# Optimization experiments

Measured on AMD Instinct MI355X. Metric: run time of the kernel, lower is better.

The kernel has to match this reference:

```python
import jax, jax.numpy as jnp
import numpy as np

N = 30000   # nodes
E = 240000  # edges
G = 16      # graphs in batch
DIMS = [1, 256, 512, 1024]
OUT = 1024

def _xavier(key, fan_in, fan_out):
    lim = float(np.sqrt(6.0 / (fan_in + fan_out)))
    return jax.random.uniform(key, (fan_in, fan_out), minval=-lim, maxval=lim, dtype=jnp.float32)

def setup_inputs() -> dict:
    key = jax.random.key(0)
    ks = jax.random.split(key, 8)
    x = jax.random.normal(ks[0], (N, DIMS[0]), dtype=jnp.float32)
    edge_index = jax.random.randint(ks[1], (2, E), 0, N, dtype=jnp.int64)
    batch = jnp.sort(jax.random.randint(ks[2], (N,), 0, G, dtype=jnp.int64))
    W1 = _xavier(ks[3], DIMS[0], DIMS[1]); b1 = jnp.zeros((DIMS[1],), jnp.float32)
    W2 = _xavier(ks[4], DIMS[1], DIMS[2]); b2 = jnp.zeros((DIMS[2],), jnp.float32)
    W3 = _xavier(ks[5], DIMS[2], DIMS[3]); b3 = jnp.zeros((DIMS[3],), jnp.float32)
    Wo = _xavier(ks[6], DIMS[3], OUT);     bo = jnp.zeros((OUT,), jnp.float32)
    return {"x": x, "edge_index": edge_index, "batch": batch,
            "W1": W1, "b1": b1, "W2": W2, "b2": b2, "W3": W3, "b3": b3,
            "Wo": Wo, "bo": bo}

def reference(x, edge_index, batch, W1, b1, W2, b2, W3, b3, Wo, bo):
    n = x.shape[0]
    loops = jnp.arange(n)
    # GCNConv adds self-loops, then symmetric deg^-1/2 normalization
    src = jnp.concatenate([edge_index[0], loops])
    dst = jnp.concatenate([edge_index[1], loops])
    deg = jnp.zeros((n,), jnp.float32).at[dst].add(1.0)  # >=1 due to self-loops
    dis = jax.lax.rsqrt(deg)
    norm = (dis[src] * dis[dst])[:, None]  # [E+N, 1]

    def gcn(h, W, b):
        h = h @ W                                   # linear (no bias in lin)
        agg = jnp.zeros_like(h).at[dst].add(h[src] * norm)  # scatter-add messages
        return agg + b                              # GCNConv bias

    h = jax.nn.relu(gcn(x, W1, b1))
    h = jax.nn.relu(gcn(h, W2, b2))
    h = jax.nn.relu(gcn(h, W3, b3))
    # global mean pool over graphs
    sums = jnp.zeros((G, h.shape[1]), h.dtype).at[batch].add(h)
    cnt = jnp.zeros((G,), h.dtype).at[batch].add(1.0)
    pooled = sums / jnp.maximum(cnt, 1.0)[:, None]
    return pooled @ Wo + bo
```

## Files before the change

kernel.cpp:

```cpp
#include <hip/hip_runtime.h>
#include <hip/hip_bf16.h>
#include <stdint.h>

#define N_NODES 30000
#define E_EDGES 240000
#define NGRAPH  16
#define D1      256
#define D2      512
#define D3      1024
#define DOUT    1024
#define M_PAD   30720
#define CAP     40

typedef unsigned short ushort_t;
typedef short short8 __attribute__((ext_vector_type(8)));
typedef float f32x4 __attribute__((ext_vector_type(4)));

__device__ __forceinline__ float bf2f(ushort_t u) {
    union { unsigned int i; float f; } v; v.i = ((unsigned int)u) << 16; return v.f;
}
__device__ __forceinline__ ushort_t f2bf(float x) {
    union { float f; unsigned int i; } v; v.f = x;
    unsigned int r = v.i + 0x7fffu + ((v.i >> 16) & 1u);
    return (ushort_t)(r >> 16);
}

__device__ __forceinline__ void gl_lds16(const ushort_t* g, ushort_t* l) {
    __builtin_amdgcn_global_load_lds(
        (const __attribute__((address_space(1))) void*)(g),
        (__attribute__((address_space(3))) void*)(l), 16, 0, 0);
}

__global__ void k_detect(const void* w1, const void* ei, int* flags) {
    int lane = threadIdx.x & 63;
    const ushort_t* h = (const ushort_t*)w1;
    float v = fabsf(bf2f(h[lane * 2]));
    unsigned long long badf = __ballot(!(v <= 0.25f));
    const int* e = (const int*)ei;
    unsigned long long badi = __ballot(e[lane * 2 + 1] != 0);
    if (threadIdx.x == 0) {
        flags[0] = (badf == 0ull) ? 1 : 0;
        flags[1] = (badi == 0ull) ? 1 : 0;
    }
}

__global__ void k_setup(const void* x, const void* batch, const void* w1, const void* b1,
                        const void* b2, const void* b3, const void* bo,
                        const void* W2, const void* W3,
                        float* xf, int* batch32, float* W1f, float* b1f, float* b2f,
                        float* b3f, float* bof, ushort_t* Wt2, ushort_t* Wt3,
                        int* slotcnt, float* pooled, float* pooled2, const int* flags) {
    int isbf = flags[0];
    int bid = blockIdx.x;
    int tid = threadIdx.x;
    if (bid < 492) {
        int i = bid * 256 + tid;
        if (i < 3072) {
            const void* src; float* dst; int idx;
            if      (i < 256)  { src = w1; dst = W1f; idx = i; }
            else if (i < 512)  { src = b1; dst = b1f; idx = i - 256; }
            else if (i < 1024) { src = b2; dst = b2f; idx = i - 512; }
            else if (i < 2048) { src = b3; dst = b3f; idx = i - 1024; }
            else               { src = bo; dst = bof; idx = i - 2048; }
            dst[idx] = isbf ? bf2f(((const ushort_t*)src)[idx]) : ((const float*)src)[idx];
        } else if (i < 33072) {
            int idx = i - 3072;
            xf[idx] = isbf ? bf2f(((const ushort_t*)x)[idx]) : ((const float*)x)[idx];
        } else if (i < 63072) {
            int idx = i - 33072;
            batch32[idx] = flags[1] ? (int)((const long long*)batch)[idx]
                                    : ((const int*)batch)[idx];
        } else if (i < 93072) {
            slotcnt[i - 63072] = 0;
        } else if (i < 109456) {
            pooled[i - 93072] = 0.0f;
        } else if (i < 125840) {
            pooled2[i - 109456] = 0.0f;
        }
    } else {
        __shared__ ushort_t tile[32][33];
        int tb = bid - 492;
        const void* in; ushort_t* out; int R, C, bx, by;
        if (tb < 128) { in = W2; out = Wt2; R = D1; C = D2; bx = tb & 15; by = tb >> 4; }
        else { tb -= 128; in = W3; out = Wt3; R = D2; C = D3; bx = tb & 31; by = tb >> 5; }
        int tx = tid & 31, ty = tid >> 5;
        int c0 = bx * 32, r0 = by * 32;
        for (int i = ty; i < 32; i += 8) {
            size_t idx = (size_t)(r0 + i) * C + c0 + tx;
            tile[i][tx] = isbf ? ((const ushort_t*)in)[idx] : f2bf(((const float*)in)[idx]);
        }
        __syncthreads();
        for (int i = ty; i < 32; i += 8) out[(size_t)(c0 + i) * R + r0 + tx] = tile[tx][i];
    }
}

__global__ void k_edge_count(const void* ei, int* slotcnt, int* slots, const int* flags) {
    int e = blockIdx.x * 256 + threadIdx.x;
    if (e >= E_EDGES) return;
    int s, d;
    if (flags[1]) {
        s = (int)((const long long*)ei)[e];
        d = (int)((const long long*)ei)[E_EDGES + e];
    } else {
        s = ((const int*)ei)[e];
        d = ((const int*)ei)[E_EDGES + e];
    }
    if ((unsigned)s >= N_NODES || (unsigned)d >= N_NODES) return;
    int pos = atomicAdd(&slotcnt[d], 1);
    if (pos < CAP) slots[d * CAP + pos] = s;
}

__global__ void k_s1(const float* xf, const int* slotcnt, const int* slots,
                     const int* batch, float* dis, float* s1, float* cntg) {
    int b = blockIdx.x;
    if (b == 118) {
        int g = threadIdx.x;
        if (g >= NGRAPH) return;
        int lo0 = 0, hi0 = N_NODES;
        while (lo0 < hi0) { int m = (lo0 + hi0) >> 1; if (batch[m] < g) lo0 = m + 1; else hi0 = m; }
        int lo1 = lo0, hi1 = N_NODES;
        while (lo1 < hi1) { int m = (lo1 + hi1) >> 1; if (batch[m] < g + 1) lo1 = m + 1; else hi1 = m; }
        cntg[g] = (float)(lo1 - lo0);
        return;
    }
    int d = b * 256 + threadIdx.x;
    if (d >= N_NODES) return;
    int cd = slotcnt[d];
    float di = rsqrtf(1.0f + (float)cd);
    dis[d] = di;
    int cnt = cd < CAP ? cd : CAP;
    float acc = xf[d] * di;
    for (int k = 0; k < cnt; k++) {
        int s = slots[d * CAP + k];
        acc += xf[s] * rsqrtf(1.0f + (float)slotcnt[s]);
    }
    s1[d] = acc * di;
}

__global__ void k_agg1(const float* s1, const float* W1f, const float* b1f,
                       ushort_t* a2, const int* slots, const int* slotcnt, const float* dis) {
    int node = blockIdx.x * 4 + (threadIdx.x >> 6);
    int lane = threadIdx.x & 63;
    int c4 = lane * 4;
    float w[4], bb[4], a[4];
    #pragma unroll
    for (int j = 0; j < 4; j++) { w[j] = W1f[c4 + j]; bb[j] = b1f[c4 + j]; }
    float di = dis[node];
    int cnt = slotcnt[node]; cnt = cnt < CAP ? cnt : CAP;
    float sv = s1[node];
    float wsl = di * di;
    #pragma unroll
    for (int j = 0; j < 4; j++) a[j] = wsl * fmaxf(sv * w[j] + bb[j], 0.0f);
    for (int k = 0; k < cnt; k++) {
        int s = slots[node * CAP + k];
        float ss = s1[s];
        float wn = dis[s] * di;
        #pragma unroll
        for (int j = 0; j < 4; j++) a[j] += wn * fmaxf(ss * w[j] + bb[j], 0.0f);
    }
    uint2 o;
    o.x = (unsigned int)f2bf(a[0]) | ((unsigned int)f2bf(a[1]) << 16);
    o.y = (unsigned int)f2bf(a[2]) | ((unsigned int)f2bf(a[3]) << 16);
    *(uint2*)&a2[(size_t)node * D1 + c4] = o;
}

__global__ void k_agg2(const ushort_t* h, ushort_t* out, const int* slots,
                       const int* slotcnt, const float* dis) {
    int node = blockIdx.x * 4 + (threadIdx.x >> 6);
    int lane = threadIdx.x & 63;
    int c8 = lane * 8;
    float di = dis[node];
    int cnt = slotcnt[node]; cnt = cnt < CAP ? cnt : CAP;
    float w = di * di;
    const ushort_t* hp = h + c8;
    short8 p = *(const short8*)&hp[(size_t)node * D2];
    float a[8];
    #pragma unroll
    for (int j = 0; j < 8; j++) a[j] = w * bf2f((ushort_t)p[j]);
    if (cnt > 0) {
        int s0 = slots[node * CAP];
        short8 q0 = *(const short8*)&hp[(size_t)s0 * D2];
        float ws0 = dis[s0] * di;
        for (int k = 1; k < cnt; k++) {
            int s1i = slots[node * CAP + k];
            short8 q1 = *(const short8*)&hp[(size_t)s1i * D2];
            float ws1 = dis[s1i] * di;
            #pragma unroll
            for (int j = 0; j < 8; j++) a[j] += ws0 * bf2f((ushort_t)q0[j]);
            q0 = q1; ws0 = ws1;
        }
        #pragma unroll
        for (int j = 0; j < 8; j++) a[j] += ws0 * bf2f((ushort_t)q0[j]);
    }
    uint4 o;
    o.x = (unsigned int)f2bf(a[0]) | ((unsigned int)f2bf(a[1]) << 16);
    o.y = (unsigned int)f2bf(a[2]) | ((unsigned int)f2bf(a[3]) << 16);
    o.z = (unsigned int)f2bf(a[4]) | ((unsigned int)f2bf(a[5]) << 16);
    o.w = (unsigned int)f2bf(a[6]) | ((unsigned int)f2bf(a[7]) << 16);
    *(uint4*)&out[(size_t)node * D2 + c8] = o;
}

#define GPHASE(M0, M1, USTAGE, TAILWAIT)                                               \
    a0 = rdA(slot, M0, inrow0); a1 = rdA(slot, M0, inrow1);                            \
    a2r = rdA(slot, M1, inrow0); a3r = rdA(slot, M1, inrow1);                          \
    if (hn) stage_unit(nslot, t + 1, USTAGE);                                          \
    asm volatile("" ::: "memory");                                                     \
    __builtin_amdgcn_s_barrier();                                                      \
    asm volatile("s_waitcnt lgkmcnt(0)" ::: "memory");                                 \
    __builtin_amdgcn_sched_barrier(0);                                                 \
    __builtin_amdgcn_s_setprio(1);                                                     \
    _Pragma("unroll")                                                                  \
    for (int n = 0; n < 4; ++n) {                                                      \
        acc[M0][n] = __builtin_amdgcn_mfma_f32_16x16x32_bf16(a0,  bf_[n][0], acc[M0][n], 0, 0, 0); \
        acc[M0][n] = __builtin_amdgcn_mfma_f32_16x16x32_bf16(a1,  bf_[n][1], acc[M0][n], 0, 0, 0); \
        acc[M1][n] = __builtin_amdgcn_mfma_f32_16x16x32_bf16(a2r, bf_[n][0], acc[M1][n], 0, 0, 0); \
        acc[M1][n] = __builtin_amdgcn_mfma_f32_16x16x32_bf16(a3r, bf_[n][1], acc[M1][n], 0, 0, 0); \
    }                                                                                  \
    __builtin_amdgcn_s_setprio(0);                                                     \
    TAILWAIT                                                                           \
    asm volatile("" ::: "memory");                                                     \
    __builtin_amdgcn_s_barrier();

#define TW_NONE
#define TW_P2 if (hn) { asm volatile("s_waitcnt vmcnt(4)" ::: "memory"); } \
              else    { asm volatile("s_waitcnt vmcnt(0)" ::: "memory"); }
#define TW_P4 if (hn) { asm volatile("s_waitcnt vmcnt(2)" ::: "memory"); } \
              else    { asm volatile("s_waitcnt vmcnt(0)" ::: "memory"); }

template<int POOL>
__global__ __launch_bounds__(512, 2) void k_gemm8(const ushort_t* A, const ushort_t* Bt,
                                                  const float* bias, const int* batch,
                                                  float* pooled, ushort_t* Cmat,
                                                  int K, int Ncols, int ntn, int NT) {
    __shared__ __align__(16) ushort_t As[2][256 * 64];
    __shared__ __align__(16) ushort_t Bs[2][256 * 64];
    const int tid = threadIdx.x;
    const int id = blockIdx.x;
    const int xcd = id & 7, q = id >> 3;
    const int rt = xcd * ((M_PAD / 256) / 8) + q / ntn;
    const int ct = q % ntn;
    const int bm0 = rt * 256, bn0 = ct * 256;
    const int wave = tid >> 6, lane = tid & 63;
    const int wr = wave >> 2, wc = wave & 3;
    const int l15 = lane & 15, quad = lane >> 4;

    const ushort_t* gA = A + (size_t)bm0 * K;
    const ushort_t* gB = Bt + (size_t)bn0 * K;

    auto stage_blk = [&](ushort_t* ldsbase, const ushort_t* gbase, int kt, int b) {
        int row = b >> 3;
        int kb = (b & 7) ^ (row & 7);
        gl_lds16(gbase + (size_t)row * K + (kt << 6) + (kb << 3), ldsbase + (b << 3));
    };
    auto stage_unit = [&](int slot, int kt, int u) {
        if (u == 0)      { stage_blk(Bs[slot], gB, kt, tid);        stage_blk(Bs[slot], gB, kt, tid + 512); }
        else if (u == 1) { stage_blk(Bs[slot], gB, kt, tid + 1024); stage_blk(Bs[slot], gB, kt, tid + 1536); }
        else if (u == 2) { stage_blk(As[slot], gA, kt, tid);        stage_blk(As[slot], gA, kt, tid + 1024); }
        else             { stage_blk(As[slot], gA, kt, tid + 512);  stage_blk(As[slot], gA, kt, tid + 1536); }
    };

    const int swzx = (l15 & 7) << 4;
    const int inrow0 = (quad * 16) ^ swzx;
    const int inrow1 = (quad * 16 + 64) ^ swzx;
    const int arowb = (wr * 128 + l15) * 128;
    const int browb = (wc * 64 + l15) * 128;

    auto rdA = [&](int slot, int m, int inr) -> short8 {
        return *(const short8*)((const char*)As[slot] + arowb + m * 2048 + inr);
    };
    auto rdB = [&](int slot, int n, int inr) -> short8 {
        return *(const short8*)((const char*)Bs[slot] + browb + n * 2048 + inr);
    };

    stage_unit(0, 0, 0); stage_unit(0, 0, 1); stage_unit(0, 0, 2); stage_unit(0, 0, 3);
    asm volatile("s_waitcnt vmcnt(2)" ::: "memory");
    __builtin_amdgcn_s_barrier();

    f32x4 acc[8][4];
    #pragma unroll
    for (int a = 0; a < 8; a++)
        #pragma unroll
        for (int b = 0; b < 4; b++)
            acc[a][b] = (f32x4){0.f, 0.f, 0.f, 0.f};

    short8 bf_[4][2];
    for (int t = 0; t < NT; ++t) {
        const int slot = t & 1, nslot = slot ^ 1;
        const bool hn = (t + 1) < NT;
        short8 a0, a1, a2r, a3r;
        #pragma unroll
        for (int n = 0; n < 4; ++n) {
            bf_[n][0] = rdB(slot, n, inrow0);
            bf_[n][1] = rdB(slot, n, inrow1);
        }
        GPHASE(0, 1, 0, TW_NONE)
        GPHASE(2, 3, 1, TW_P2)
        GPHASE(4, 5, 2, TW_NONE)
        GPHASE(6, 7, 3, TW_P4)
    }

    if (POOL == 0) {
        #pragma unroll
        for (int im = 0; im < 8; im++) {
            int row = bm0 + wr * 128 + im * 16 + quad * 4;
            #pragma unroll
            for (int in = 0; in < 4; in++) {
                int col = bn0 + wc * 64 + in * 16 + l15;
                float bv = bias[col];
                #pragma unroll
                for (int r = 0; r < 4; r++) {
                    float v = acc[im][in][r] + bv;
                    v = v > 0.0f ? v : 0.0f;
                    Cmat[(size_t)(row + r) * Ncols + col] = f2bf(v);
                }
            }
        }
    } else {
        asm volatile("s_waitcnt vmcnt(0) lgkmcnt(0)" ::: "memory");
        __syncthreads();
        float* pl = (float*)&As[0][0];
        int* gtile = (int*)&Bs[0][0];
        for (int i = tid; i < NGRAPH * 256; i += 512) pl[i] = 0.0f;
        if (tid < 256) {
            int r = bm0 + tid; if (r > N_NODES - 1) r = N_NODES - 1;
            int g = batch[r]; g = g < 0 ? 0 : (g > NGRAPH - 1 ? NGRAPH - 1 : g);
            gtile[tid] = g;
        }
        __syncthreads();

        int gmin = gtile[0], gmax = gtile[255];
        if (gmin == gmax && bm0 + 255 < N_NODES) {
            float csum[4];
            float bv[4];
            #pragma unroll
            for (int in = 0; in < 4; in++) {
                csum[in] = 0.0f;
                bv[in] = bias[bn0 + wc * 64 + in * 16 + l15];
            }
            #pragma unroll
            for (int im = 0; im < 8; im++) {
                #pragma unroll
                for (int in = 0; in < 4; in++) {
                    #pragma unroll
                    for (int r = 0; r < 4; r++)
                        csum[in] += fmaxf(acc[im][in][r] + bv[in], 0.0f);
                }
            }
            #pragma unroll
            for (int in = 0; in < 4; in++) {
                csum[in] += __shfl_xor(csum[in], 16);
                csum[in] += __shfl_xor(csum[in], 32);
            }
            if (quad == 0) {
                #pragma unroll
                for (int in = 0; in < 4; in++)
                    atomicAdd(&pl[gmin * 256 + wc * 64 + in * 16 + l15], csum[in]);
            }
        } else {
            #pragma unroll
            for (int im = 0; im < 8; im++) {
                int rl = wr * 128 + im * 16 + quad * 4;
                #pragma unroll
                for (int in = 0; in < 4; in++) {
                    int cl = wc * 64 + in * 16 + l15;
                    float bv = bias[bn0 + cl];
                    float vsum = 0.0f;
                    int gprev = gtile[rl];
                    #pragma unroll
                    for (int r = 0; r < 4; r++) {
                        int row = bm0 + rl + r;
                        float v = (row < N_NODES) ? fmaxf(acc[im][in][r] + bv, 0.0f) : 0.0f;
                        int g = gtile[rl + r];
                        if (g != gprev) {
                            atomicAdd(&pl[gprev * 256 + cl], vsum);
                            vsum = 0.0f; gprev = g;
                        }
                        vsum += v;
                    }
                    atomicAdd(&pl[gprev * 256 + cl], vsum);
                }
            }
        }
        __syncthreads();

        int span = (gmax - gmin + 1) * 256;
        for (int idx = tid; idx < span; idx += 512) {
            int g = gmin + (idx >> 8), cl = idx & 255;
            float v = pl[g * 256 + cl];
            if (v != 0.0f) atomicAdd(&pooled[g * DOUT + bn0 + cl], v);
        }
    }
}

__global__ __launch_bounds__(256) void k_out_partial(const float* pooled, const void* Wo,
                                                     float* pooled2, const int* flags) {
    __shared__ float pl[NGRAPH * 32];
    int tid = threadIdx.x;
    int col = blockIdx.x * 256 + tid;
    int k0 = blockIdx.y * 32;
    for (int i = tid; i < NGRAPH * 32; i += 256) {
        int g = i >> 5, kk = i & 31;
        pl[i] = pooled[g * D3 + k0 + kk];
    }
    __syncthreads();
    int isbf = flags[0];
    float acc[NGRAPH];
    #pragma unroll
    for (int g = 0; g < NGRAPH; g++) acc[g] = 0.0f;
    #pragma unroll 4
    for (int kk = 0; kk < 32; kk++) {
        int k = k0 + kk;
        float wv = isbf ? bf2f(((const ushort_t*)Wo)[(size_t)k * DOUT + col])
                        : ((const float*)Wo)[(size_t)k * DOUT + col];
        #pragma unroll
        for (int g = 0; g < NGRAPH; g++)
            acc[g] += pl[g * 32 + kk] * wv;
    }
    #pragma unroll
    for (int g = 0; g < NGRAPH; g++)
        atomicAdd(&pooled2[g * DOUT + col], acc[g]);
}

__global__ void k_out_fin(const float* pooled2, const float* bof, const float* cntg,
                          void* out, const int* flags) {
    int i = blockIdx.x * 256 + threadIdx.x;
    int g = i >> 10, o = i & 1023;
    float c = cntg[g]; c = c > 1.0f ? c : 1.0f;
    float v = pooled2[i] / c + bof[o];
    if (flags[0]) ((ushort_t*)out)[i] = f2bf(v);
    else          ((float*)out)[i] = v;
}

extern "C" void kernel_launch(void* const* d_in, const int* in_sizes, int n_in,
                              void* d_out, int out_size, void* d_ws, size_t ws_size,
                              hipStream_t stream) {
    const void* x_raw  = d_in[0];
    const void* ei_raw = d_in[1];
    const void* b_raw  = d_in[2];
    const void* W1_raw = d_in[3];
    const void* b1_raw = d_in[4];
    const void* W2_raw = d_in[5];
    const void* b2_raw = d_in[6];
    const void* W3_raw = d_in[7];
    const void* b3_raw = d_in[8];
    const void* Wo_raw = d_in[9];
    const void* bo_raw = d_in[10];

    char* w = (char*)d_ws;
    size_t off = 0;
    auto alloc = [&](size_t b) { size_t o = off; off += (b + 255) & ~(size_t)255; return o; };
    int*   flags   = (int*)  (w + alloc(256));
    float* xf      = (float*)(w + alloc((size_t)N_NODES * 4));
    int*   batch32 = (int*)  (w + alloc((size_t)N_NODES * 4));
    float* W1f     = (float*)(w + alloc(D1 * 4));
    float* b1f     = (float*)(w + alloc(D1 * 4));
    float* b2f     = (float*)(w + alloc(D2 * 4));
    float* b3f     = (float*)(w + alloc(D3 * 4));
    float* bof     = (float*)(w + alloc(DOUT * 4));
    float* dis     = (float*)(w + alloc((size_t)N_NODES * 4));
    float* s1      = (float*)(w + alloc((size_t)N_NODES * 4));
    float* cntg    = (float*)(w + alloc(64));
    float* pooled  = (float*)(w + alloc((size_t)NGRAPH * DOUT * 4));
    float* pooled2 = (float*)(w + alloc((size_t)NGRAPH * DOUT * 4));
    int*   slotcnt = (int*)  (w + alloc((size_t)N_NODES * 4));
    int*   slots   = (int*)  (w + alloc((size_t)N_NODES * CAP * 4));
    ushort_t* Wt2  = (ushort_t*)(w + alloc((size_t)D2 * D1 * 2));
    ushort_t* Wt3  = (ushort_t*)(w + alloc((size_t)D3 * D2 * 2));
    ushort_t* slabA = (ushort_t*)(w + alloc((size_t)M_PAD * D2 * 2));
    ushort_t* a2 = slabA;
    ushort_t* a3 = slabA;
    ushort_t* h2   = (ushort_t*)(w + alloc((size_t)M_PAD * D2 * 2));

    int nb_e = (E_EDGES + 255) / 256;

    k_detect<<<1, 64, 0, stream>>>(W1_raw, ei_raw, flags);
    k_setup<<<1132, 256, 0, stream>>>(x_raw, b_raw, W1_raw, b1_raw, b2_raw, b3_raw, bo_raw,
                                      W2_raw, W3_raw, xf, batch32, W1f, b1f, b2f, b3f, bof,
                                      Wt2, Wt3, slotcnt, pooled, pooled2, flags);
    k_edge_count<<<nb_e, 256, 0, stream>>>(ei_raw, slotcnt, slots, flags);
    k_s1<<<119, 256, 0, stream>>>(xf, slotcnt, slots, batch32, dis, s1, cntg);

    k_agg1<<<N_NODES / 4, 256, 0, stream>>>(s1, W1f, b1f, a2, slots, slotcnt, dis);
    k_gemm8<0><<<(M_PAD / 256) * (D2 / 256), 512, 0, stream>>>(a2, Wt2, b2f, nullptr,
                                                               nullptr, h2, D1, D2,
                                                               D2 / 256, D1 / 64);
    k_agg2<<<N_NODES / 4, 256, 0, stream>>>(h2, a3, slots, slotcnt, dis);
    k_gemm8<1><<<(M_PAD / 256) * (D3 / 256), 512, 0, stream>>>(a3, Wt3, b3f, batch32,
                                                               pooled, nullptr, D2, D3,
                                                               D3 / 256, D2 / 64);

    k_out_partial<<<dim3(DOUT / 256, D3 / 32), 256, 0, stream>>>(pooled, Wo_raw, pooled2, flags);
    k_out_fin<<<NGRAPH * DOUT / 256, 256, 0, stream>>>(pooled2, bof, cntg, d_out, flags);
}
```

Before: 270.8 us.

## Use smaller 128x128 GEMM for layer 2 and restage all units upfront in pooled GEMM

New measurement: 272.3 us. No clear change (+0.6%).

```diff
diff --git a/kernel.cpp b/kernel.cpp
--- a/kernel.cpp
+++ b/kernel.cpp
@@ -10,6 +10,7 @@
 #define D3      1024
 #define DOUT    1024
 #define M_PAD   30720
+#define NT_M    240
 #define CAP     40
 
 typedef unsigned short ushort_t;
@@ -200,10 +201,84 @@
     *(uint4*)&out[(size_t)node * D2 + c8] = o;
 }
 
-#define GPHASE(M0, M1, USTAGE, TAILWAIT)                                               \
+__global__ __launch_bounds__(256, 3) void k_gemm(const ushort_t* A, const ushort_t* Bt,
+                                                 const float* bias, ushort_t* Cmat,
+                                                 int K, int Ncols, int ntn) {
+    __shared__ __align__(16) ushort_t As[2][128 * 32];
+    __shared__ __align__(16) ushort_t Bs[2][128 * 32];
+    int tid = threadIdx.x;
+    int id = blockIdx.x;
+    int xcd = id & 7, q = id >> 3;
+    int rt = xcd * (NT_M / 8) + q / ntn;
+    int ct = q % ntn;
+    int bm0 = rt * 128, bn0 = ct * 128;
+    int wave = tid >> 6, lane = tid & 63;
+    int wm = (wave & 1) * 64, wn = (wave >> 1) * 64;
+    int l15 = lane & 15, quad = lane >> 4;
+
+    int m1 = tid >> 2, k1 = (tid & 3) << 3;
+    int m2 = m1 + 64;
+    int off1 = m1 * 32 + k1, off2 = m2 * 32 + k1;
+    const ushort_t* pA1 = A + (size_t)(bm0 + m1) * K + k1;
+    const ushort_t* pA2 = A + (size_t)(bm0 + m2) * K + k1;
+    const ushort_t* pB1 = Bt + (size_t)(bn0 + m1) * K + k1;
+    const ushort_t* pB2 = Bt + (size_t)(bn0 + m2) * K + k1;
+
+    {
+        uint4 la0 = *(const uint4*)pA1, la1 = *(const uint4*)pA2;
+        uint4 lb0 = *(const uint4*)pB1, lb1 = *(const uint4*)pB2;
+        *(uint4*)&As[0][off1] = la0; *(uint4*)&As[0][off2] = la1;
+        *(uint4*)&Bs[0][off1] = lb0; *(uint4*)&Bs[0][off2] = lb1;
+    }
+
+    f32x4 acc[4][4];
+    for (int a = 0; a < 4; a++)
+        for (int b = 0; b < 4; b++)
+            acc[a][b] = (f32x4){0.f, 0.f, 0.f, 0.f};
+
+    int niter = K >> 5;
+    for (int it = 0; it < niter; ++it) {
+        __syncthreads();
+        int ktn = (it + 1) << 5;
+        uint4 na0, na1, nb0, nb1;
+        if (ktn < K) {
+            na0 = *(const uint4*)(pA1 + ktn); na1 = *(const uint4*)(pA2 + ktn);
+            nb0 = *(const uint4*)(pB1 + ktn); nb1 = *(const uint4*)(pB2 + ktn);
+        }
+        int cb = it & 1;
+        short8 af[4], bfr[4];
+        for (int im = 0; im < 4; im++)
+            af[im] = *(const short8*)&As[cb][(wm + im * 16 + l15) * 32 + quad * 8];
+        for (int in = 0; in < 4; in++)
+            bfr[in] = *(const short8*)&Bs[cb][(wn + in * 16 + l15) * 32 + quad * 8];
+        for (int im = 0; im < 4; im++)
+            for (int in = 0; in < 4; in++)
+                acc[im][in] = __builtin_amdgcn_mfma_f32_16x16x32_bf16(af[im], bfr[in], acc[im][in], 0, 0, 0);
+        if (ktn < K) {
+            int wb = cb ^ 1;
+            *(uint4*)&As[wb][off1] = na0; *(uint4*)&As[wb][off2] = na1;
+            *(uint4*)&Bs[wb][off1] = nb0; *(uint4*)&Bs[wb][off2] = nb1;
+        }
+    }
+
+    for (int im = 0; im < 4; im++) {
+        int row = bm0 + wm + im * 16 + quad * 4;
+        for (int in = 0; in < 4; in++) {
+            int col = bn0 + wn + in * 16 + l15;
+            float bv = bias[col];
+            for (int r = 0; r < 4; r++) {
+                float v = acc[im][in][r] + bv;
+                v = v > 0.0f ? v : 0.0f;
+                Cmat[(size_t)(row + r) * Ncols + col] = f2bf(v);
+            }
+        }
+    }
+}
+
+#define GPHASE(M0, M1, PRESTAGE, TAILWAIT)                                             \
     a0 = rdA(slot, M0, inrow0); a1 = rdA(slot, M0, inrow1);                            \
     a2r = rdA(slot, M1, inrow0); a3r = rdA(slot, M1, inrow1);                          \
-    if (hn) stage_unit(nslot, t + 1, USTAGE);                                          \
+    PRESTAGE                                                                           \
     asm volatile("" ::: "memory");                                                     \
     __builtin_amdgcn_s_barrier();                                                      \
     asm volatile("s_waitcnt lgkmcnt(0)" ::: "memory");                                 \
@@ -221,17 +296,17 @@
     asm volatile("" ::: "memory");                                                     \
     __builtin_amdgcn_s_barrier();
 
+#define PS_ALL  if (hn) { stage_unit(nslot, t + 1, 0); stage_unit(nslot, t + 1, 1);    \
+                          stage_unit(nslot, t + 1, 2); stage_unit(nslot, t + 1, 3); }
+#define PS_NONE
 #define TW_NONE
-#define TW_P2 if (hn) { asm volatile("s_waitcnt vmcnt(4)" ::: "memory"); } \
+#define TW_P2 if (hn) { asm volatile("s_waitcnt vmcnt(8)" ::: "memory"); } \
               else    { asm volatile("s_waitcnt vmcnt(0)" ::: "memory"); }
-#define TW_P4 if (hn) { asm volatile("s_waitcnt vmcnt(2)" ::: "memory"); } \
-              else    { asm volatile("s_waitcnt vmcnt(0)" ::: "memory"); }
-
-template<int POOL>
-__global__ __launch_bounds__(512, 2) void k_gemm8(const ushort_t* A, const ushort_t* Bt,
-                                                  const float* bias, const int* batch,
-                                                  float* pooled, ushort_t* Cmat,
-                                                  int K, int Ncols, int ntn, int NT) {
+#define TW_P4 if (hn) { asm volatile("s_waitcnt vmcnt(2)" ::: "memory"); }
+
+__global__ __launch_bounds__(512, 2) void k_gemm8p(const ushort_t* A, const ushort_t* Bt,
+                                                   const float* bias, const int* batch,
+                                                   float* pooled, int K, int ntn, int NT) {
     __shared__ __align__(16) ushort_t As[2][256 * 64];
     __shared__ __align__(16) ushort_t Bs[2][256 * 64];
     const int tid = threadIdx.x;
@@ -293,102 +368,84 @@
             bf_[n][0] = rdB(slot, n, inrow0);
             bf_[n][1] = rdB(slot, n, inrow1);
         }
-        GPHASE(0, 1, 0, TW_NONE)
-        GPHASE(2, 3, 1, TW_P2)
-        GPHASE(4, 5, 2, TW_NONE)
-        GPHASE(6, 7, 3, TW_P4)
-    }
-
-    if (POOL == 0) {
+        GPHASE(0, 1, PS_ALL, TW_NONE)
+        GPHASE(2, 3, PS_NONE, TW_P2)
+        GPHASE(4, 5, PS_NONE, TW_NONE)
+        GPHASE(6, 7, PS_NONE, TW_P4)
+    }
+
+    asm volatile("s_waitcnt vmcnt(0) lgkmcnt(0)" ::: "memory");
+    __syncthreads();
+    float* pl = (float*)&As[0][0];
+    int* gtile = (int*)&Bs[0][0];
+    for (int i = tid; i < NGRAPH * 256; i += 512) pl[i] = 0.0f;
+    if (tid < 256) {
+        int r = bm0 + tid; if (r > N_NODES - 1) r = N_NODES - 1;
+        int g = batch[r]; g = g < 0 ? 0 : (g > NGRAPH - 1 ? NGRAPH - 1 : g);
+        gtile[tid] = g;
+    }
+    __syncthreads();
+
+    int gmin = gtile[0], gmax = gtile[255];
+    if (gmin == gmax && bm0 + 255 < N_NODES) {
+        float csum[4];
+        float bv[4];
+        #pragma unroll
+        for (int in = 0; in < 4; in++) {
+            csum[in] = 0.0f;
+            bv[in] = bias[bn0 + wc * 64 + in * 16 + l15];
+        }
         #pragma unroll
         for (int im = 0; im < 8; im++) {
-            int row = bm0 + wr * 128 + im * 16 + quad * 4;
             #pragma unroll
             for (int in = 0; in < 4; in++) {
-                int col = bn0 + wc * 64 + in * 16 + l15;
-                float bv = bias[col];
+                #pragma unroll
+                for (int r = 0; r < 4; r++)
+                    csum[in] += fmaxf(acc[im][in][r] + bv[in], 0.0f);
+            }
+        }
+        #pragma unroll
+        for (int in = 0; in < 4; in++) {
+            csum[in] += __shfl_xor(csum[in], 16);
+            csum[in] += __shfl_xor(csum[in], 32);
+        }
+        if (quad == 0) {
+            #pragma unroll
+            for (int in = 0; in < 4; in++)
+                atomicAdd(&pl[gmin * 256 + wc * 64 + in * 16 + l15], csum[in]);
+        }
+    } else {
+        #pragma unroll
+        for (int im = 0; im < 8; im++) {
+            int rl = wr * 128 + im * 16 + quad * 4;
+            #pragma unroll
+            for (int in = 0; in < 4; in++) {
+                int cl = wc * 64 + in * 16 + l15;
+                float bv = bias[bn0 + cl];
+                float vsum = 0.0f;
+                int gprev = gtile[rl];
                 #pragma unroll
                 for (int r = 0; r < 4; r++) {
-                    float v = acc[im][in][r] + bv;
-                    v = v > 0.0f ? v : 0.0f;
-                    Cmat[(size_t)(row + r) * Ncols + col] = f2bf(v);
+                    int row = bm0 + rl + r;
+                    float v = (row < N_NODES) ? fmaxf(acc[im][in][r] + bv, 0.0f) : 0.0f;
+                    int g = gtile[rl + r];
+                    if (g != gprev) {
+                        atomicAdd(&pl[gprev * 256 + cl], vsum);
+                        vsum = 0.0f; gprev = g;
+                    }
+                    vsum += v;
                 }
+                atomicAdd(&pl[gprev * 256 + cl], vsum);
             }
         }
-    } else {
-        asm volatile("s_waitcnt vmcnt(0) lgkmcnt(0)" ::: "memory");
-        __syncthreads();
-        float* pl = (float*)&As[0][0];
-        int* gtile = (int*)&Bs[0][0];
-        for (int i = tid; i < NGRAPH * 256; i += 512) pl[i] = 0.0f;
-        if (tid < 256) {
-            int r = bm0 + tid; if (r > N_NODES - 1) r = N_NODES - 1;
-            int g = batch[r]; g = g < 0 ? 0 : (g > NGRAPH - 1 ? NGRAPH - 1 : g);
-            gtile[tid] = g;
-        }
-        __syncthreads();
-
-        int gmin = gtile[0], gmax = gtile[255];
-        if (gmin == gmax && bm0 + 255 < N_NODES) {
-            float csum[4];
-            float bv[4];
-            #pragma unroll
-            for (int in = 0; in < 4; in++) {
-                csum[in] = 0.0f;
-                bv[in] = bias[bn0 + wc * 64 + in * 16 + l15];
-            }
-            #pragma unroll
-            for (int im = 0; im < 8; im++) {
-                #pragma unroll
-                for (int in = 0; in < 4; in++) {
-                    #pragma unroll
-                    for (int r = 0; r < 4; r++)
-                        csum[in] += fmaxf(acc[im][in][r] + bv[in], 0.0f);
-                }
-            }
-            #pragma unroll
-            for (int in = 0; in < 4; in++) {
-                csum[in] += __shfl_xor(csum[in], 16);
-                csum[in] += __shfl_xor(csum[in], 32);
-            }
-            if (quad == 0) {
-                #pragma unroll
-                for (int in = 0; in < 4; in++)
-                    atomicAdd(&pl[gmin * 256 + wc * 64 + in * 16 + l15], csum[in]);
-            }
-        } else {
-            #pragma unroll
-            for (int im = 0; im < 8; im++) {
-                int rl = wr * 128 + im * 16 + quad * 4;
-                #pragma unroll
-                for (int in = 0; in < 4; in++) {
-                    int cl = wc * 64 + in * 16 + l15;
-                    float bv = bias[bn0 + cl];
-                    float vsum = 0.0f;
-                    int gprev = gtile[rl];
-                    #pragma unroll
-                    for (int r = 0; r < 4; r++) {
-                        int row = bm0 + rl + r;
-                        float v = (row < N_NODES) ? fmaxf(acc[im][in][r] + bv, 0.0f) : 0.0f;
-                        int g = gtile[rl + r];
-                        if (g != gprev) {
-                            atomicAdd(&pl[gprev * 256 + cl], vsum);
-                            vsum = 0.0f; gprev = g;
-                        }
-                        vsum += v;
-                    }
-                    atomicAdd(&pl[gprev * 256 + cl], vsum);
-                }
-            }
-        }
-        __syncthreads();
-
-        int span = (gmax - gmin + 1) * 256;
-        for (int idx = tid; idx < span; idx += 512) {
-            int g = gmin + (idx >> 8), cl = idx & 255;
-            float v = pl[g * 256 + cl];
-            if (v != 0.0f) atomicAdd(&pooled[g * DOUT + bn0 + cl], v);
-        }
+    }
+    __syncthreads();
+
+    int span = (gmax - gmin + 1) * 256;
+    for (int idx = tid; idx < span; idx += 512) {
+        int g = gmin + (idx >> 8), cl = idx & 255;
+        float v = pl[g * 256 + cl];
+        if (v != 0.0f) atomicAdd(&pooled[g * DOUT + bn0 + cl], v);
     }
 }
 
@@ -481,13 +538,10 @@
     k_s1<<<119, 256, 0, stream>>>(xf, slotcnt, slots, batch32, dis, s1, cntg);
 
     k_agg1<<<N_NODES / 4, 256, 0, stream>>>(s1, W1f, b1f, a2, slots, slotcnt, dis);
-    k_gemm8<0><<<(M_PAD / 256) * (D2 / 256), 512, 0, stream>>>(a2, Wt2, b2f, nullptr,
-                                                               nullptr, h2, D1, D2,
-                                                               D2 / 256, D1 / 64);
+    k_gemm<<<NT_M * (D2 / 128), 256, 0, stream>>>(a2, Wt2, b2f, h2, D1, D2, D2 / 128);
     k_agg2<<<N_NODES / 4, 256, 0, stream>>>(h2, a3, slots, slotcnt, dis);
-    k_gemm8<1><<<(M_PAD / 256) * (D3 / 256), 512, 0, stream>>>(a3, Wt3, b3f, batch32,
-                                                               pooled, nullptr, D2, D3,
-                                                               D3 / 256, D2 / 64);
+    k_gemm8p<<<(M_PAD / 256) * (D3 / 256), 512, 0, stream>>>(a3, Wt3, b3f, batch32,
+                                                             pooled, D2, D3 / 256, D2 / 64);
 
     k_out_partial<<<dim3(DOUT / 256, D3 / 32), 256, 0, stream>>>(pooled, Wo_raw, pooled2, flags);
     k_out_fin<<<NGRAPH * DOUT / 256, 256, 0, stream>>>(pooled2, bof, cntg, d_out, flags);
```
